# Kernel tuning notes

Measured on AMD Instinct MI355X. Metric: run time of the kernel, lower is better.

Reference implementation:

```python
import jax, jax.numpy as jnp
import numpy as np

B, S, D, H, DFF = 2, 2048, 2048, 16, 8192
DH = D // H
EPS = 1e-5


def _layer_norm(x, g, b):
    mu = jnp.mean(x, axis=-1, keepdims=True)
    var = jnp.mean(jnp.square(x - mu), axis=-1, keepdims=True)
    return (x - mu) * jax.lax.rsqrt(var + EPS) * g + b


def setup_inputs() -> dict:
    key = jax.random.key(0)
    ks = jax.random.split(key, 12)
    sc = 0.02
    inp = {
        "x": jax.random.normal(ks[0], (B, S, D), dtype=jnp.float32),
        # attention projections, stored [in, out] (torch Linear weight transposed)
        "wq": jax.random.normal(ks[1], (D, D), dtype=jnp.float32) * sc,
        "bq": jnp.zeros((D,), jnp.float32),
        "wk": jax.random.normal(ks[2], (D, D), dtype=jnp.float32) * sc,
        "bk": jnp.zeros((D,), jnp.float32),
        "wv": jax.random.normal(ks[3], (D, D), dtype=jnp.float32) * sc,
        "bv": jnp.zeros((D,), jnp.float32),
        "wo": jax.random.normal(ks[4], (D, D), dtype=jnp.float32) * sc,
        "bo": jnp.zeros((D,), jnp.float32),
        "ln1_g": jnp.ones((D,), jnp.float32),
        "ln1_b": jnp.zeros((D,), jnp.float32),
        # feed-forward
        "w1": jax.random.normal(ks[5], (D, DFF), dtype=jnp.float32) * sc,
        "b1": jnp.zeros((DFF,), jnp.float32),
        "w2": jax.random.normal(ks[6], (DFF, D), dtype=jnp.float32) * sc,
        "b2": jnp.zeros((D,), jnp.float32),
        "ln2_g": jnp.ones((D,), jnp.float32),
        "ln2_b": jnp.zeros((D,), jnp.float32),
    }
    return inp


def reference(x, wq, bq, wk, bk, wv, bv, wo, bo, ln1_g, ln1_b,
              w1, b1, w2, b2, ln2_g, ln2_b):
    # ---- MultiHeadAttentionBlock: x + MHA(LN(x)) ----
    h = _layer_norm(x, ln1_g, ln1_b)                      # [B,S,D]
    q = (h @ wq + bq).reshape(B, S, H, DH).transpose(0, 2, 1, 3)  # [B,H,S,DH]
    k = (h @ wk + bk).reshape(B, S, H, DH).transpose(0, 2, 1, 3)
    v = (h @ wv + bv).reshape(B, S, H, DH).transpose(0, 2, 1, 3)

    # faithful to source: scale by sqrt(d_dim), NOT sqrt(head_dim)
    scores = jnp.einsum("bhqd,bhkd->bhqk", q, k) / np.sqrt(D).astype(np.float32)
    # faithful triu/transpose masking (softmax sees raw zeros, not -inf)
    t = jnp.triu(scores).swapaxes(-2, -1)                 # [B,H,S,S]
    s = jax.nn.softmax(t, axis=-2)
    r = jnp.triu(s).swapaxes(-2, -1)
    attn = jnp.einsum("bhqk,bhkd->bhqd", r, v)            # [B,H,S,DH]
    attn = attn.transpose(0, 2, 1, 3).reshape(B, S, D)
    x = x + attn @ wo + bo

    # ---- FeedForwardBlock: x + FF(LN(x)), dropout rate 0 ----
    h2 = _layer_norm(x, ln2_g, ln2_b)
    ff = jax.nn.relu(h2 @ w1 + b1) @ w2 + b2
    return x + ff
```

## Files before the change

kernel.cpp:

```cpp
#include <hip/hip_runtime.h>


typedef unsigned short ushort_t;
typedef unsigned int   uint32;
typedef __attribute__((ext_vector_type(8))) short    short8;
typedef __attribute__((ext_vector_type(8))) ushort_t ushort8;
typedef __attribute__((ext_vector_type(4))) float    f32x4;

#define BDIM   2
#define SEQ    2048
#define DMODEL 2048
#define NHEAD  16
#define DHEAD  128
#define DFFN   8192
#define MROWS  (BDIM*SEQ)
#define LDQKV  6144

#define GPTR(p) (const __attribute__((address_space(1))) void*)((const void*)(p))
#define SPTR(p) (__attribute__((address_space(3))) void*)((void*)(p))

__device__ __forceinline__ float bf2f(ushort_t u) {
  union { uint32 i; float f; } c; c.i = ((uint32)u) << 16; return c.f;
}
__device__ __forceinline__ ushort_t f2bf(float f) {
  union { float f; uint32 i; } c; c.f = f;
  uint32 u = c.i;
  return (ushort_t)((u + 0x7fffu + ((u >> 16) & 1u)) >> 16);
}

__global__ __launch_bounds__(256) void transpose_f32_bf16_kern(
    const float* __restrict__ W, ushort_t* __restrict__ Wt, int K, int N)
{
  __shared__ float tile[32][33];
  const int nb = blockIdx.x * 32, kb = blockIdx.y * 32;
  const int tx = threadIdx.x & 31, ty = threadIdx.x >> 5;
#pragma unroll
  for (int j = 0; j < 32; j += 8)
    tile[ty + j][tx] = W[(size_t)(kb + ty + j) * N + nb + tx];
  __syncthreads();
#pragma unroll
  for (int j = 0; j < 32; j += 8)
    Wt[(size_t)(nb + ty + j) * K + kb + tx] = f2bf(tile[tx][ty + j]);
}

__global__ __launch_bounds__(256) void bias_concat_kern(
    const float* __restrict__ a, const float* __restrict__ b,
    const float* __restrict__ c, float* __restrict__ o)
{
  const int i = blockIdx.x * 256 + threadIdx.x;
  o[i] = (i < 2048) ? a[i] : ((i < 4096) ? b[i - 2048] : c[i - 4096]);
}

__global__ __launch_bounds__(256) void ln_kern(
    const float* __restrict__ X, const float* __restrict__ G,
    const float* __restrict__ Bb, ushort_t* __restrict__ Out)
{
  const int row = blockIdx.x, tid = threadIdx.x;
  const float* xr = X + (size_t)row * DMODEL;
  float4 v0 = ((const float4*)xr)[tid * 2];
  float4 v1 = ((const float4*)xr)[tid * 2 + 1];
  float s  = v0.x + v0.y + v0.z + v0.w + v1.x + v1.y + v1.z + v1.w;
  float ss = v0.x*v0.x + v0.y*v0.y + v0.z*v0.z + v0.w*v0.w
           + v1.x*v1.x + v1.y*v1.y + v1.z*v1.z + v1.w*v1.w;
#pragma unroll
  for (int off = 32; off > 0; off >>= 1) {
    s  += __shfl_down(s, off);
    ss += __shfl_down(ss, off);
  }
  __shared__ float rs[4], rss[4];
  __shared__ float sh_mu, sh_rst;
  const int wv = tid >> 6;
  if ((tid & 63) == 0) { rs[wv] = s; rss[wv] = ss; }
  __syncthreads();
  if (tid == 0) {
    float S1 = rs[0] + rs[1] + rs[2] + rs[3];
    float S2 = rss[0] + rss[1] + rss[2] + rss[3];
    float mu = S1 * (1.f / DMODEL);
    float var = S2 * (1.f / DMODEL) - mu * mu;
    sh_mu = mu;
    sh_rst = rsqrtf(var + 1e-5f);
  }
  __syncthreads();
  const float mu = sh_mu, rst = sh_rst;
  float4 g0 = ((const float4*)G)[tid * 2];
  float4 g1 = ((const float4*)G)[tid * 2 + 1];
  float4 b0 = ((const float4*)Bb)[tid * 2];
  float4 b1 = ((const float4*)Bb)[tid * 2 + 1];
  ushort8 o;
  o[0] = f2bf((v0.x - mu) * rst * g0.x + b0.x);
  o[1] = f2bf((v0.y - mu) * rst * g0.y + b0.y);
  o[2] = f2bf((v0.z - mu) * rst * g0.z + b0.z);
  o[3] = f2bf((v0.w - mu) * rst * g0.w + b0.w);
  o[4] = f2bf((v1.x - mu) * rst * g1.x + b1.x);
  o[5] = f2bf((v1.y - mu) * rst * g1.y + b1.y);
  o[6] = f2bf((v1.z - mu) * rst * g1.z + b1.z);
  o[7] = f2bf((v1.w - mu) * rst * g1.w + b1.w);
  *(ushort8*)(Out + (size_t)row * DMODEL + tid * 8) = o;
}

template<int OUT, int RELU, int RESID, int KDIV>
__global__ __launch_bounds__(512, 2) void gemm8_kern(
    const ushort_t* __restrict__ A, const ushort_t* __restrict__ Bt,
    const float* __restrict__ bias, const float* __restrict__ resid,
    void* __restrict__ Cout, int M, int N, int K)
{
  __shared__ ushort_t sA[4 * 8192];
  __shared__ ushort_t sB[4 * 8192];

  const int tid = threadIdx.x;
  const int nM  = gridDim.y;
  const int nwg = gridDim.x * nM;
  const int bid = blockIdx.y * gridDim.x + blockIdx.x;
  const int cpx = nwg >> 3;
  const int swz = (bid & 7) * cpx + (bid >> 3);
  const int m0 = (swz % nM) * 256;
  const int n0 = (swz / nM) * 256;

  const int Keff = K / KDIV;
  const int k0 = (KDIV > 1) ? blockIdx.z * Keff : 0;
  const int T = Keff >> 6;

  const int l = tid & 63, w = tid >> 6;
  const int lr = l & 15, lg = l >> 4;
  const int wr = w >> 2, wc = w & 3;

  const int xch   = (lg ^ ((lr >> 1) & 3)) * 8;
  const int abase = (wr * 128 + lr) * 32 + xch;
  const int bbase = (wc * 64  + lr) * 32 + xch;

  const int sr = tid >> 2;
  const int sg = ((tid & 3) ^ ((tid >> 3) & 3)) * 8;
  const ushort_t* Asrc = A  + (size_t)(m0 + sr) * K + k0 + sg;
  const ushort_t* Bsrc = Bt + (size_t)(n0 + sr) * K + k0 + sg;
  ushort_t* dA = sA + tid * 8;
  ushort_t* dB = sB + tid * 8;

#define SA_(slot, kt, kk, r) __builtin_amdgcn_global_load_lds( \
    GPTR(Asrc + (size_t)(r) * 128 * K + (kt) * 64 + (kk) * 32), \
    SPTR(dA + (slot) * 8192 + (r) * 4096), 16, 0, 0)
#define SB_(slot, kt, kk, r) __builtin_amdgcn_global_load_lds( \
    GPTR(Bsrc + (size_t)(r) * 128 * K + (kt) * 64 + (kk) * 32), \
    SPTR(dB + (slot) * 8192 + (r) * 4096), 16, 0, 0)

  f32x4 acc[8][4] = {};

  SA_(0, 0, 0, 0); SA_(0, 0, 0, 1); SB_(0, 0, 0, 0); SB_(0, 0, 0, 1);
  SA_(1, 0, 1, 0); SA_(1, 0, 1, 1); SB_(1, 0, 1, 0); SB_(1, 0, 1, 1);
  SA_(2, 1, 0, 0); SA_(2, 1, 0, 1); SB_(2, 1, 0, 0); SB_(2, 1, 0, 1);
  asm volatile("s_waitcnt vmcnt(8)" ::: "memory");
  __builtin_amdgcn_s_barrier();

  for (int t = 0; t < T; ++t) {
    const int c = t & 1;
    const ushort_t* A0 = sA + (c * 2 + 0) * 8192;
    const ushort_t* B0 = sB + (c * 2 + 0) * 8192;
    const ushort_t* A1 = sA + (c * 2 + 1) * 8192;
    const ushort_t* B1 = sB + (c * 2 + 1) * 8192;
    const int s1 = (c ^ 1) * 2 + 1;
    const int s0 = c * 2;
    const bool pf1 = (t + 1 < T), pf0 = (t + 2 < T);
    const bool last2 = (t >= T - 2);

    short8 a0, a1, a2, a3, b0, b1, b2, b3;

    b0 = *(const short8*)(B0 + bbase);
    b1 = *(const short8*)(B0 + bbase + 512);
    b2 = *(const short8*)(B0 + bbase + 1024);
    b3 = *(const short8*)(B0 + bbase + 1536);
    a0 = *(const short8*)(A0 + abase);
    a1 = *(const short8*)(A0 + abase + 512);
    a2 = *(const short8*)(A0 + abase + 1024);
    a3 = *(const short8*)(A0 + abase + 1536);
    if (pf1) { SA_(s1, t + 1, 1, 0); SA_(s1, t + 1, 1, 1); }
    __builtin_amdgcn_s_barrier();
    asm volatile("s_waitcnt lgkmcnt(0)" ::: "memory");
    __builtin_amdgcn_sched_barrier(0);
    __builtin_amdgcn_s_setprio(1);
    acc[0][0] = __builtin_amdgcn_mfma_f32_16x16x32_bf16(a0, b0, acc[0][0], 0, 0, 0);
    acc[0][1] = __builtin_amdgcn_mfma_f32_16x16x32_bf16(a0, b1, acc[0][1], 0, 0, 0);
    acc[0][2] = __builtin_amdgcn_mfma_f32_16x16x32_bf16(a0, b2, acc[0][2], 0, 0, 0);
    acc[0][3] = __builtin_amdgcn_mfma_f32_16x16x32_bf16(a0, b3, acc[0][3], 0, 0, 0);
    acc[1][0] = __builtin_amdgcn_mfma_f32_16x16x32_bf16(a1, b0, acc[1][0], 0, 0, 0);
    acc[1][1] = __builtin_amdgcn_mfma_f32_16x16x32_bf16(a1, b1, acc[1][1], 0, 0, 0);
    acc[1][2] = __builtin_amdgcn_mfma_f32_16x16x32_bf16(a1, b2, acc[1][2], 0, 0, 0);
    acc[1][3] = __builtin_amdgcn_mfma_f32_16x16x32_bf16(a1, b3, acc[1][3], 0, 0, 0);
    acc[2][0] = __builtin_amdgcn_mfma_f32_16x16x32_bf16(a2, b0, acc[2][0], 0, 0, 0);
    acc[2][1] = __builtin_amdgcn_mfma_f32_16x16x32_bf16(a2, b1, acc[2][1], 0, 0, 0);
    acc[2][2] = __builtin_amdgcn_mfma_f32_16x16x32_bf16(a2, b2, acc[2][2], 0, 0, 0);
    acc[2][3] = __builtin_amdgcn_mfma_f32_16x16x32_bf16(a2, b3, acc[2][3], 0, 0, 0);
    acc[3][0] = __builtin_amdgcn_mfma_f32_16x16x32_bf16(a3, b0, acc[3][0], 0, 0, 0);
    acc[3][1] = __builtin_amdgcn_mfma_f32_16x16x32_bf16(a3, b1, acc[3][1], 0, 0, 0);
    acc[3][2] = __builtin_amdgcn_mfma_f32_16x16x32_bf16(a3, b2, acc[3][2], 0, 0, 0);
    acc[3][3] = __builtin_amdgcn_mfma_f32_16x16x32_bf16(a3, b3, acc[3][3], 0, 0, 0);
    __builtin_amdgcn_s_setprio(0);
    __builtin_amdgcn_s_barrier();

    a0 = *(const short8*)(A0 + abase + 2048);
    a1 = *(const short8*)(A0 + abase + 2560);
    a2 = *(const short8*)(A0 + abase + 3072);
    a3 = *(const short8*)(A0 + abase + 3584);
    if (pf1) { SB_(s1, t + 1, 1, 0); SB_(s1, t + 1, 1, 1); }
    __builtin_amdgcn_s_barrier();
    asm volatile("s_waitcnt lgkmcnt(0)" ::: "memory");
    __builtin_amdgcn_sched_barrier(0);
    __builtin_amdgcn_s_setprio(1);
    acc[4][0] = __builtin_amdgcn_mfma_f32_16x16x32_bf16(a0, b0, acc[4][0], 0, 0, 0);
    acc[4][1] = __builtin_amdgcn_mfma_f32_16x16x32_bf16(a0, b1, acc[4][1], 0, 0, 0);
    acc[4][2] = __builtin_amdgcn_mfma_f32_16x16x32_bf16(a0, b2, acc[4][2], 0, 0, 0);
    acc[4][3] = __builtin_amdgcn_mfma_f32_16x16x32_bf16(a0, b3, acc[4][3], 0, 0, 0);
    acc[5][0] = __builtin_amdgcn_mfma_f32_16x16x32_bf16(a1, b0, acc[5][0], 0, 0, 0);
    acc[5][1] = __builtin_amdgcn_mfma_f32_16x16x32_bf16(a1, b1, acc[5][1], 0, 0, 0);
    acc[5][2] = __builtin_amdgcn_mfma_f32_16x16x32_bf16(a1, b2, acc[5][2], 0, 0, 0);
    acc[5][3] = __builtin_amdgcn_mfma_f32_16x16x32_bf16(a1, b3, acc[5][3], 0, 0, 0);
    acc[6][0] = __builtin_amdgcn_mfma_f32_16x16x32_bf16(a2, b0, acc[6][0], 0, 0, 0);
    acc[6][1] = __builtin_amdgcn_mfma_f32_16x16x32_bf16(a2, b1, acc[6][1], 0, 0, 0);
    acc[6][2] = __builtin_amdgcn_mfma_f32_16x16x32_bf16(a2, b2, acc[6][2], 0, 0, 0);
    acc[6][3] = __builtin_amdgcn_mfma_f32_16x16x32_bf16(a2, b3, acc[6][3], 0, 0, 0);
    acc[7][0] = __builtin_amdgcn_mfma_f32_16x16x32_bf16(a3, b0, acc[7][0], 0, 0, 0);
    acc[7][1] = __builtin_amdgcn_mfma_f32_16x16x32_bf16(a3, b1, acc[7][1], 0, 0, 0);
    acc[7][2] = __builtin_amdgcn_mfma_f32_16x16x32_bf16(a3, b2, acc[7][2], 0, 0, 0);
    acc[7][3] = __builtin_amdgcn_mfma_f32_16x16x32_bf16(a3, b3, acc[7][3], 0, 0, 0);
    __builtin_amdgcn_s_setprio(0);
    if (!last2) { asm volatile("s_waitcnt vmcnt(8)" ::: "memory"); }
    else        { asm volatile("s_waitcnt vmcnt(0)" ::: "memory"); }
    __builtin_amdgcn_s_barrier();

    b0 = *(const short8*)(B1 + bbase);
    b1 = *(const short8*)(B1 + bbase + 512);
    b2 = *(const short8*)(B1 + bbase + 1024);
    b3 = *(const short8*)(B1 + bbase + 1536);
    a0 = *(const short8*)(A1 + abase);
    a1 = *(const short8*)(A1 + abase + 512);
    a2 = *(const short8*)(A1 + abase + 1024);
    a3 = *(const short8*)(A1 + abase + 1536);
    if (pf0) { SA_(s0, t + 2, 0, 0); SA_(s0, t + 2, 0, 1); }
    __builtin_amdgcn_s_barrier();
    asm volatile("s_waitcnt lgkmcnt(0)" ::: "memory");
    __builtin_amdgcn_sched_barrier(0);
    __builtin_amdgcn_s_setprio(1);
    acc[0][0] = __builtin_amdgcn_mfma_f32_16x16x32_bf16(a0, b0, acc[0][0], 0, 0, 0);
    acc[0][1] = __builtin_amdgcn_mfma_f32_16x16x32_bf16(a0, b1, acc[0][1], 0, 0, 0);
    acc[0][2] = __builtin_amdgcn_mfma_f32_16x16x32_bf16(a0, b2, acc[0][2], 0, 0, 0);
    acc[0][3] = __builtin_amdgcn_mfma_f32_16x16x32_bf16(a0, b3, acc[0][3], 0, 0, 0);
    acc[1][0] = __builtin_amdgcn_mfma_f32_16x16x32_bf16(a1, b0, acc[1][0], 0, 0, 0);
    acc[1][1] = __builtin_amdgcn_mfma_f32_16x16x32_bf16(a1, b1, acc[1][1], 0, 0, 0);
    acc[1][2] = __builtin_amdgcn_mfma_f32_16x16x32_bf16(a1, b2, acc[1][2], 0, 0, 0);
    acc[1][3] = __builtin_amdgcn_mfma_f32_16x16x32_bf16(a1, b3, acc[1][3], 0, 0, 0);
    acc[2][0] = __builtin_amdgcn_mfma_f32_16x16x32_bf16(a2, b0, acc[2][0], 0, 0, 0);
    acc[2][1] = __builtin_amdgcn_mfma_f32_16x16x32_bf16(a2, b1, acc[2][1], 0, 0, 0);
    acc[2][2] = __builtin_amdgcn_mfma_f32_16x16x32_bf16(a2, b2, acc[2][2], 0, 0, 0);
    acc[2][3] = __builtin_amdgcn_mfma_f32_16x16x32_bf16(a2, b3, acc[2][3], 0, 0, 0);
    acc[3][0] = __builtin_amdgcn_mfma_f32_16x16x32_bf16(a3, b0, acc[3][0], 0, 0, 0);
    acc[3][1] = __builtin_amdgcn_mfma_f32_16x16x32_bf16(a3, b1, acc[3][1], 0, 0, 0);
    acc[3][2] = __builtin_amdgcn_mfma_f32_16x16x32_bf16(a3, b2, acc[3][2], 0, 0, 0);
    acc[3][3] = __builtin_amdgcn_mfma_f32_16x16x32_bf16(a3, b3, acc[3][3], 0, 0, 0);
    __builtin_amdgcn_s_setprio(0);
    __builtin_amdgcn_s_barrier();

    a0 = *(const short8*)(A1 + abase + 2048);
    a1 = *(const short8*)(A1 + abase + 2560);
    a2 = *(const short8*)(A1 + abase + 3072);
    a3 = *(const short8*)(A1 + abase + 3584);
    if (pf0) { SB_(s0, t + 2, 0, 0); SB_(s0, t + 2, 0, 1); }
    __builtin_amdgcn_s_barrier();
    asm volatile("s_waitcnt lgkmcnt(0)" ::: "memory");
    __builtin_amdgcn_sched_barrier(0);
    __builtin_amdgcn_s_setprio(1);
    acc[4][0] = __builtin_amdgcn_mfma_f32_16x16x32_bf16(a0, b0, acc[4][0], 0, 0, 0);
    acc[4][1] = __builtin_amdgcn_mfma_f32_16x16x32_bf16(a0, b1, acc[4][1], 0, 0, 0);
    acc[4][2] = __builtin_amdgcn_mfma_f32_16x16x32_bf16(a0, b2, acc[4][2], 0, 0, 0);
    acc[4][3] = __builtin_amdgcn_mfma_f32_16x16x32_bf16(a0, b3, acc[4][3], 0, 0, 0);
    acc[5][0] = __builtin_amdgcn_mfma_f32_16x16x32_bf16(a1, b0, acc[5][0], 0, 0, 0);
    acc[5][1] = __builtin_amdgcn_mfma_f32_16x16x32_bf16(a1, b1, acc[5][1], 0, 0, 0);
    acc[5][2] = __builtin_amdgcn_mfma_f32_16x16x32_bf16(a1, b2, acc[5][2], 0, 0, 0);
    acc[5][3] = __builtin_amdgcn_mfma_f32_16x16x32_bf16(a1, b3, acc[5][3], 0, 0, 0);
    acc[6][0] = __builtin_amdgcn_mfma_f32_16x16x32_bf16(a2, b0, acc[6][0], 0, 0, 0);
    acc[6][1] = __builtin_amdgcn_mfma_f32_16x16x32_bf16(a2, b1, acc[6][1], 0, 0, 0);
    acc[6][2] = __builtin_amdgcn_mfma_f32_16x16x32_bf16(a2, b2, acc[6][2], 0, 0, 0);
    acc[6][3] = __builtin_amdgcn_mfma_f32_16x16x32_bf16(a2, b3, acc[6][3], 0, 0, 0);
    acc[7][0] = __builtin_amdgcn_mfma_f32_16x16x32_bf16(a3, b0, acc[7][0], 0, 0, 0);
    acc[7][1] = __builtin_amdgcn_mfma_f32_16x16x32_bf16(a3, b1, acc[7][1], 0, 0, 0);
    acc[7][2] = __builtin_amdgcn_mfma_f32_16x16x32_bf16(a3, b2, acc[7][2], 0, 0, 0);
    acc[7][3] = __builtin_amdgcn_mfma_f32_16x16x32_bf16(a3, b3, acc[7][3], 0, 0, 0);
    __builtin_amdgcn_s_setprio(0);
    if (!last2) { asm volatile("s_waitcnt vmcnt(8)" ::: "memory"); }
    else        { asm volatile("s_waitcnt vmcnt(0)" ::: "memory"); }
    __builtin_amdgcn_s_barrier();
  }
#undef SA_
#undef SB_

  ushort_t* Pz = (OUT == 2)
      ? (ushort_t*)Cout + (size_t)blockIdx.z * M * N : (ushort_t*)Cout;
#pragma unroll
  for (int mi = 0; mi < 8; ++mi) {
#pragma unroll
    for (int ni = 0; ni < 4; ++ni) {
      const int gn = n0 + wc * 64 + ni * 16 + lr;
      const float bvv = (OUT == 2) ? 0.f : bias[gn];
#pragma unroll
      for (int j = 0; j < 4; ++j) {
        const int gm = m0 + wr * 128 + mi * 16 + lg * 4 + j;
        float v = acc[mi][ni][j] + bvv;
        if (RESID) v += resid[(size_t)gm * N + gn];
        if (RELU) v = fmaxf(v, 0.f);
        if (OUT == 0)      ((float*)Cout)[(size_t)gm * N + gn] = v;
        else               Pz[(size_t)gm * N + gn] = f2bf(v);
      }
    }
  }
}

__global__ __launch_bounds__(256) void combine_kern(
    const ushort_t* __restrict__ pp, const float* __restrict__ bias,
    const float* __restrict__ resid, float* __restrict__ out)
{
  const size_t i = ((size_t)blockIdx.x * 256 + threadIdx.x) * 8;
  ushort8 p0 = *(const ushort8*)(pp + i);
  ushort8 p1 = *(const ushort8*)(pp + (size_t)MROWS * 2048 + i);
  const int col = (int)(i & 2047);
  float4 r0 = *(const float4*)(resid + i);
  float4 r1 = *(const float4*)(resid + i + 4);
  float4 c0 = *(const float4*)(bias + col);
  float4 c1 = *(const float4*)(bias + col + 4);
  float4 o0, o1;
  o0.x = bf2f(p0[0]) + bf2f(p1[0]) + c0.x + r0.x;
  o0.y = bf2f(p0[1]) + bf2f(p1[1]) + c0.y + r0.y;
  o0.z = bf2f(p0[2]) + bf2f(p1[2]) + c0.z + r0.z;
  o0.w = bf2f(p0[3]) + bf2f(p1[3]) + c0.w + r0.w;
  o1.x = bf2f(p0[4]) + bf2f(p1[4]) + c1.x + r1.x;
  o1.y = bf2f(p0[5]) + bf2f(p1[5]) + c1.y + r1.y;
  o1.z = bf2f(p0[6]) + bf2f(p1[6]) + c1.z + r1.z;
  o1.w = bf2f(p0[7]) + bf2f(p1[7]) + c1.w + r1.w;
  *(float4*)(out + i) = o0;
  *(float4*)(out + i + 4) = o1;
}

__global__ __launch_bounds__(256) void attn_stats_kern(
    const ushort_t* __restrict__ Q, const ushort_t* __restrict__ Kb,
    float* __restrict__ E, float* __restrict__ DG, int ld)
{
  __shared__ ushort_t Ksm[64 * 128];
  const int qb = blockIdx.x;
  const int bh = blockIdx.y;
  const int b = bh >> 4, h = bh & 15;
  const int tid = threadIdx.x;
  const int l = tid & 63, w = tid >> 6;
  const int lr = l & 15, lg = l >> 4;

  const int qrow0 = qb * 64 + w * 16;

  const size_t qoff = (size_t)(b * SEQ + qrow0 + lr) * ld + h * DHEAD + lg * 8;
  short8 af[4];
#pragma unroll
  for (int c = 0; c < 4; ++c) af[c] = *(const short8*)(Q + qoff + c * 32);

  const int srow_b = w * 16 + (l >> 4);
  const ushort_t* Kg = Kb + (size_t)b * SEQ * ld + (size_t)h * DHEAD;
  ushort_t* Sbase = Ksm + w * 2048;

  f32x4 sume = {0.f, 0.f, 0.f, 0.f};
  f32x4 dge  = {0.f, 0.f, 0.f, 0.f};
  const float scale = 0.0220970869120796f;
  const int rx = lr & 7;

  for (int kc = qb; kc < 32; ++kc) {
    __syncthreads();
#pragma unroll
    for (int c = 0; c < 4; ++c) {
      const int row = srow_b + c * 4;
      const int g = (l & 15) ^ (row & 7);
      __builtin_amdgcn_global_load_lds(
          GPTR(Kg + (size_t)(kc * 64 + row) * ld + g * 8),
          SPTR(Sbase + c * 512), 16, 0, 0);
    }
    __syncthreads();

    const int ks0 = (kc == qb) ? w : 0;
    for (int ks = ks0; ks < 4; ++ks) {
      short8 bfr[4];
#pragma unroll
      for (int c = 0; c < 4; ++c)
        bfr[c] = *(const short8*)(Ksm + (ks * 16 + lr) * 128 + ((lg + c * 4) ^ rx) * 8);
      f32x4 sc = {0.f, 0.f, 0.f, 0.f};
      sc = __builtin_amdgcn_mfma_f32_16x16x32_bf16(af[0], bfr[0], sc, 0, 0, 0);
      sc = __builtin_amdgcn_mfma_f32_16x16x32_bf16(af[1], bfr[1], sc, 0, 0, 0);
      sc = __builtin_amdgcn_mfma_f32_16x16x32_bf16(af[2], bfr[2], sc, 0, 0, 0);
      sc = __builtin_amdgcn_mfma_f32_16x16x32_bf16(af[3], bfr[3], sc, 0, 0, 0);
      if (kc == qb && ks == w) {
        const int ki = kc * 64 + ks * 16 + lr;
#pragma unroll
        for (int j = 0; j < 4; ++j) {
          const int qi = qrow0 + lg * 4 + j;
          if (ki >= qi) {
            float e = __expf(sc[j] * scale);
            sume[j] += e;
            if (ki == qi) dge[j] += e;
          }
        }
      } else {
#pragma unroll
        for (int j = 0; j < 4; ++j)
          sume[j] += __expf(sc[j] * scale);
      }
    }
  }

#pragma unroll
  for (int j = 0; j < 4; ++j) {
#pragma unroll
    for (int off = 1; off < 16; off <<= 1) {
      sume[j] += __shfl_xor(sume[j], off);
      dge[j]  += __shfl_xor(dge[j], off);
    }
  }
  if (lr == 0) {
#pragma unroll
    for (int j = 0; j < 4; ++j) {
      E[(size_t)bh * SEQ + qrow0 + lg * 4 + j]  = sume[j];
      DG[(size_t)bh * SEQ + qrow0 + lg * 4 + j] = dge[j];
    }
  }
}

__global__ __launch_bounds__(128) void vchunk_kern(
    const ushort_t* __restrict__ V, float* __restrict__ CS, int ld)
{
  const int c = blockIdx.x, bh = blockIdx.y;
  const int b = bh >> 4, h = bh & 15;
  const int dh = threadIdx.x;
  const ushort_t* vp = V + (size_t)(b * SEQ + c * 64) * ld + h * DHEAD + dh;
  float s = 0.f;
  for (int i = 0; i < 64; ++i) s += bf2f(vp[(size_t)i * ld]);
  CS[((size_t)bh * 32 + c) * 128 + dh] = s;
}

__global__ __launch_bounds__(128) void attn_combine_kern(
    const ushort_t* __restrict__ V, const float* __restrict__ CS,
    const float* __restrict__ E, const float* __restrict__ DG,
    ushort_t* __restrict__ Attn, int ldv)
{
  const int c = blockIdx.x, bh = blockIdx.y;
  const int b = bh >> 4, h = bh & 15;
  const int dh = threadIdx.x;
  float prefix = 0.f;
  for (int cc = 0; cc < c; ++cc) prefix += CS[((size_t)bh * 32 + cc) * 128 + dh];
  const ushort_t* vp = V + (size_t)(b * SEQ + c * 64) * ldv + h * DHEAD + dh;
  ushort_t* ap = Attn + (size_t)(b * SEQ + c * 64) * DMODEL + h * DHEAD + dh;
  const int qb = c * 64;
  for (int i = 0; i < 64; ++i) {
    const int qq = qb + i;
    const float denom = (float)qq + E[(size_t)bh * SEQ + qq];
    const float de = DG[(size_t)bh * SEQ + qq];
    const float vv = bf2f(vp[(size_t)i * ldv]);
    ap[(size_t)i * DMODEL] = f2bf((prefix + de * vv) / denom);
    prefix += vv;
  }
}

extern "C" void kernel_launch(void* const* d_in, const int* in_sizes, int n_in,
                              void* d_out, int out_size, void* d_ws, size_t ws_size,
                              hipStream_t stream)
{
  const float* x    = (const float*)d_in[0];
  const float* wq   = (const float*)d_in[1];
  const float* bq   = (const float*)d_in[2];
  const float* wk   = (const float*)d_in[3];
  const float* bk   = (const float*)d_in[4];
  const float* wv   = (const float*)d_in[5];
  const float* bv   = (const float*)d_in[6];
  const float* wo   = (const float*)d_in[7];
  const float* bo   = (const float*)d_in[8];
  const float* ln1g = (const float*)d_in[9];
  const float* ln1b = (const float*)d_in[10];
  const float* w1   = (const float*)d_in[11];
  const float* b1   = (const float*)d_in[12];
  const float* w2   = (const float*)d_in[13];
  const float* b2   = (const float*)d_in[14];
  const float* ln2g = (const float*)d_in[15];
  const float* ln2b = (const float*)d_in[16];
  float* out = (float*)d_out;

  char* ws = (char*)d_ws;
  ushort_t* W1T  = (ushort_t*)(ws + 0);
  ushort_t* PPf2 = (ushort_t*)(ws + 0);
  ushort_t* W2T  = (ushort_t*)(ws + 33554432);
  ushort_t* WOT  = (ushort_t*)(ws + 67108864);
  float*    X2   = (float*)   (ws + 75497472);
  float*    Bcat = (float*)   (ws + 75497472);
  ushort_t* Hb   = (ushort_t*)(ws + 109051904);
  ushort_t* F1   = (ushort_t*)(ws + 125829120);
  ushort_t* PPwo = (ushort_t*)(ws + 125829120);
  ushort_t* WQKV = (ushort_t*)(ws + 125829120);
  ushort_t* QKVb = (ushort_t*)(ws + 150994944);
  float*    Eb   = (float*)   (ws + 201326592);
  float*    DGb  = (float*)   (ws + 201588736);
  float*    CSb  = (float*)   (ws + 201850880);

  transpose_f32_bf16_kern<<<dim3(64, 64),  256, 0, stream>>>(wq, WQKV,                   2048, 2048);
  transpose_f32_bf16_kern<<<dim3(64, 64),  256, 0, stream>>>(wk, WQKV + 2048 * 2048,     2048, 2048);
  transpose_f32_bf16_kern<<<dim3(64, 64),  256, 0, stream>>>(wv, WQKV + 2 * 2048 * 2048, 2048, 2048);
  transpose_f32_bf16_kern<<<dim3(64, 64),  256, 0, stream>>>(wo, WOT, 2048, 2048);
  transpose_f32_bf16_kern<<<dim3(256, 64), 256, 0, stream>>>(w1, W1T, 2048, 8192);
  transpose_f32_bf16_kern<<<dim3(64, 256), 256, 0, stream>>>(w2, W2T, 8192, 2048);
  bias_concat_kern<<<24, 256, 0, stream>>>(bq, bk, bv, Bcat);

  ln_kern<<<MROWS, 256, 0, stream>>>(x, ln1g, ln1b, Hb);

  gemm8_kern<1, 0, 0, 1><<<dim3(24, 16), 512, 0, stream>>>(
      Hb, WQKV, Bcat, nullptr, QKVb, MROWS, LDQKV, DMODEL);

  attn_stats_kern<<<dim3(32, 32), 256, 0, stream>>>(QKVb, QKVb + 2048, Eb, DGb, LDQKV);

  vchunk_kern<<<dim3(32, 32), 128, 0, stream>>>(QKVb + 4096, CSb, LDQKV);
  attn_combine_kern<<<dim3(32, 32), 128, 0, stream>>>(QKVb + 4096, CSb, Eb, DGb, Hb, LDQKV);

  gemm8_kern<2, 0, 0, 2><<<dim3(8, 16, 2), 512, 0, stream>>>(
      Hb, WOT, bo, nullptr, PPwo, MROWS, DMODEL, DMODEL);
  combine_kern<<<4096, 256, 0, stream>>>(PPwo, bo, x, X2);

  ln_kern<<<MROWS, 256, 0, stream>>>(X2, ln2g, ln2b, Hb);

  gemm8_kern<1, 1, 0, 1><<<dim3(32, 16), 512, 0, stream>>>(
      Hb, W1T, b1, nullptr, F1, MROWS, DFFN, DMODEL);

  gemm8_kern<2, 0, 0, 2><<<dim3(8, 16, 2), 512, 0, stream>>>(
      F1, W2T, b2, nullptr, PPf2, MROWS, DMODEL, DFFN);
  combine_kern<<<4096, 256, 0, stream>>>(PPf2, b2, X2, out);
}
```

Before: 687.3 us.

## Fuse weight prep launches, fuse combine with LN2, widen attention-stats query tiles

Merges the six weight transpose launches and the bias concat into a single prep kernel. Fuses the split-K combine for the output projection with the second layer norm, so X2 is not re-read. The attention-stats kernel now processes 128 query rows per block, two 16-row groups per wave, so each loaded K tile is reused for twice as many queries. It also drops the sched_barrier calls in the GEMM main loop, which gives the compiler freedom to reorder but may disturb the hand-tuned interleaving.

```diff
diff --git a/kernel.cpp b/kernel.cpp
--- a/kernel.cpp
+++ b/kernel.cpp
@@ -3,9 +3,9 @@
 
 typedef unsigned short ushort_t;
 typedef unsigned int   uint32;
-typedef __attribute__((ext_vector_type(8))) short    short8;
-typedef __attribute__((ext_vector_type(8))) ushort_t ushort8;
-typedef __attribute__((ext_vector_type(4))) float    f32x4;
+typedef __attribute__((ext_vector_type(8)))  short    short8;
+typedef __attribute__((ext_vector_type(8)))  ushort_t ushort8;
+typedef __attribute__((ext_vector_type(4)))  float    f32x4;
 
 #define BDIM   2
 #define SEQ    2048
@@ -28,11 +28,34 @@
   return (ushort_t)((u + 0x7fffu + ((u >> 16) & 1u)) >> 16);
 }
 
-__global__ __launch_bounds__(256) void transpose_f32_bf16_kern(
-    const float* __restrict__ W, ushort_t* __restrict__ Wt, int K, int N)
-{
+__global__ __launch_bounds__(256) void prep_kern(
+    const float* __restrict__ wq, const float* __restrict__ wk,
+    const float* __restrict__ wv, const float* __restrict__ wo,
+    const float* __restrict__ w1, const float* __restrict__ w2,
+    const float* __restrict__ bq, const float* __restrict__ bk,
+    const float* __restrict__ bv,
+    ushort_t* __restrict__ WQKV, ushort_t* __restrict__ WOT,
+    ushort_t* __restrict__ W1T, ushort_t* __restrict__ W2T,
+    float* __restrict__ Bcat)
+{
+  const int bid = blockIdx.x;
+  if (bid >= 49152) {
+    for (int i = threadIdx.x; i < 6144; i += 256)
+      Bcat[i] = (i < 2048) ? bq[i] : ((i < 4096) ? bk[i - 2048] : bv[i - 4096]);
+    return;
+  }
+  const float* W; ushort_t* Wt; int K, N, local;
+  if (bid < 12288) {
+    const int which = bid >> 12; local = bid & 4095;
+    W = (which == 0) ? wq : (which == 1) ? wk : wv;
+    Wt = WQKV + (size_t)which * 2048 * 2048; K = 2048; N = 2048;
+  } else if (bid < 16384) { W = wo; Wt = WOT; K = 2048; N = 2048; local = bid - 12288; }
+  else if (bid < 32768)   { W = w1; Wt = W1T; K = 2048; N = 8192; local = bid - 16384; }
+  else                    { W = w2; Wt = W2T; K = 8192; N = 2048; local = bid - 32768; }
+  const int ntiles = N >> 5;
+  const int nb = (local % ntiles) * 32, kb = (local / ntiles) * 32;
+
   __shared__ float tile[32][33];
-  const int nb = blockIdx.x * 32, kb = blockIdx.y * 32;
   const int tx = threadIdx.x & 31, ty = threadIdx.x >> 5;
 #pragma unroll
   for (int j = 0; j < 32; j += 8)
@@ -41,14 +64,6 @@
 #pragma unroll
   for (int j = 0; j < 32; j += 8)
     Wt[(size_t)(nb + ty + j) * K + kb + tx] = f2bf(tile[tx][ty + j]);
-}
-
-__global__ __launch_bounds__(256) void bias_concat_kern(
-    const float* __restrict__ a, const float* __restrict__ b,
-    const float* __restrict__ c, float* __restrict__ o)
-{
-  const int i = blockIdx.x * 256 + threadIdx.x;
-  o[i] = (i < 2048) ? a[i] : ((i < 4096) ? b[i - 2048] : c[i - 4096]);
 }
 
 __global__ __launch_bounds__(256) void ln_kern(
@@ -98,11 +113,58 @@
   *(ushort8*)(Out + (size_t)row * DMODEL + tid * 8) = o;
 }
 
-template<int OUT, int RELU, int RESID, int KDIV>
+__global__ __launch_bounds__(256) void combine_ln_kern(
+    const ushort_t* __restrict__ pp, const float* __restrict__ bias,
+    const float* __restrict__ xres, const float* __restrict__ G,
+    const float* __restrict__ Bb, float* __restrict__ X2,
+    ushort_t* __restrict__ Out)
+{
+  const int row = blockIdx.x, tid = threadIdx.x;
+  const size_t i = (size_t)row * DMODEL + tid * 8;
+  ushort8 p0 = *(const ushort8*)(pp + i);
+  ushort8 p1 = *(const ushort8*)(pp + (size_t)MROWS * 2048 + i);
+  float v[8];
+#pragma unroll
+  for (int j = 0; j < 8; ++j)
+    v[j] = bf2f(p0[j]) + bf2f(p1[j]) + bias[tid * 8 + j] + xres[i + j];
+  float4 o0 = {v[0], v[1], v[2], v[3]}, o1 = {v[4], v[5], v[6], v[7]};
+  *(float4*)(X2 + i) = o0;
+  *(float4*)(X2 + i + 4) = o1;
+
+  float s = 0.f, ss = 0.f;
+#pragma unroll
+  for (int j = 0; j < 8; ++j) { s += v[j]; ss += v[j] * v[j]; }
+#pragma unroll
+  for (int off = 32; off > 0; off >>= 1) {
+    s  += __shfl_down(s, off);
+    ss += __shfl_down(ss, off);
+  }
+  __shared__ float rs[4], rss[4];
+  __shared__ float sh_mu, sh_rst;
+  const int wvv = tid >> 6;
+  if ((tid & 63) == 0) { rs[wvv] = s; rss[wvv] = ss; }
+  __syncthreads();
+  if (tid == 0) {
+    float S1 = rs[0] + rs[1] + rs[2] + rs[3];
+    float S2 = rss[0] + rss[1] + rss[2] + rss[3];
+    float mu = S1 * (1.f / DMODEL);
+    float var = S2 * (1.f / DMODEL) - mu * mu;
+    sh_mu = mu; sh_rst = rsqrtf(var + 1e-5f);
+  }
+  __syncthreads();
+  const float mu = sh_mu, rst = sh_rst;
+  ushort8 o;
+#pragma unroll
+  for (int j = 0; j < 8; ++j)
+    o[j] = f2bf((v[j] - mu) * rst * G[tid * 8 + j] + Bb[tid * 8 + j]);
+  *(ushort8*)(Out + i) = o;
+}
+
+template<int OUT, int RELU, int KDIV>
 __global__ __launch_bounds__(512, 2) void gemm8_kern(
     const ushort_t* __restrict__ A, const ushort_t* __restrict__ Bt,
-    const float* __restrict__ bias, const float* __restrict__ resid,
-    void* __restrict__ Cout, int M, int N, int K)
+    const float* __restrict__ bias, void* __restrict__ Cout,
+    int M, int N, int K)
 {
   __shared__ ushort_t sA[4 * 8192];
   __shared__ ushort_t sB[4 * 8192];
@@ -174,7 +236,6 @@
     if (pf1) { SA_(s1, t + 1, 1, 0); SA_(s1, t + 1, 1, 1); }
     __builtin_amdgcn_s_barrier();
     asm volatile("s_waitcnt lgkmcnt(0)" ::: "memory");
-    __builtin_amdgcn_sched_barrier(0);
     __builtin_amdgcn_s_setprio(1);
     acc[0][0] = __builtin_amdgcn_mfma_f32_16x16x32_bf16(a0, b0, acc[0][0], 0, 0, 0);
     acc[0][1] = __builtin_amdgcn_mfma_f32_16x16x32_bf16(a0, b1, acc[0][1], 0, 0, 0);
@@ -202,7 +263,6 @@
     if (pf1) { SB_(s1, t + 1, 1, 0); SB_(s1, t + 1, 1, 1); }
     __builtin_amdgcn_s_barrier();
     asm volatile("s_waitcnt lgkmcnt(0)" ::: "memory");
-    __builtin_amdgcn_sched_barrier(0);
     __builtin_amdgcn_s_setprio(1);
     acc[4][0] = __builtin_amdgcn_mfma_f32_16x16x32_bf16(a0, b0, acc[4][0], 0, 0, 0);
     acc[4][1] = __builtin_amdgcn_mfma_f32_16x16x32_bf16(a0, b1, acc[4][1], 0, 0, 0);
@@ -236,7 +296,6 @@
     if (pf0) { SA_(s0, t + 2, 0, 0); SA_(s0, t + 2, 0, 1); }
     __builtin_amdgcn_s_barrier();
     asm volatile("s_waitcnt lgkmcnt(0)" ::: "memory");
-    __builtin_amdgcn_sched_barrier(0);
     __builtin_amdgcn_s_setprio(1);
     acc[0][0] = __builtin_amdgcn_mfma_f32_16x16x32_bf16(a0, b0, acc[0][0], 0, 0, 0);
     acc[0][1] = __builtin_amdgcn_mfma_f32_16x16x32_bf16(a0, b1, acc[0][1], 0, 0, 0);
@@ -264,7 +323,6 @@
     if (pf0) { SB_(s0, t + 2, 0, 0); SB_(s0, t + 2, 0, 1); }
     __builtin_amdgcn_s_barrier();
     asm volatile("s_waitcnt lgkmcnt(0)" ::: "memory");
-    __builtin_amdgcn_sched_barrier(0);
     __builtin_amdgcn_s_setprio(1);
     acc[4][0] = __builtin_amdgcn_mfma_f32_16x16x32_bf16(a0, b0, acc[4][0], 0, 0, 0);
     acc[4][1] = __builtin_amdgcn_mfma_f32_16x16x32_bf16(a0, b1, acc[4][1], 0, 0, 0);
@@ -302,10 +360,8 @@
       for (int j = 0; j < 4; ++j) {
         const int gm = m0 + wr * 128 + mi * 16 + lg * 4 + j;
         float v = acc[mi][ni][j] + bvv;
-        if (RESID) v += resid[(size_t)gm * N + gn];
         if (RELU) v = fmaxf(v, 0.f);
-        if (OUT == 0)      ((float*)Cout)[(size_t)gm * N + gn] = v;
-        else               Pz[(size_t)gm * N + gn] = f2bf(v);
+        Pz[(size_t)gm * N + gn] = f2bf(v);
       }
     }
   }
@@ -348,23 +404,26 @@
   const int l = tid & 63, w = tid >> 6;
   const int lr = l & 15, lg = l >> 4;
 
-  const int qrow0 = qb * 64 + w * 16;
-
-  const size_t qoff = (size_t)(b * SEQ + qrow0 + lr) * ld + h * DHEAD + lg * 8;
-  short8 af[4];
-#pragma unroll
-  for (int c = 0; c < 4; ++c) af[c] = *(const short8*)(Q + qoff + c * 32);
+  const int qrow0 = qb * 128 + w * 32;
+
+  short8 af[2][4];
+#pragma unroll
+  for (int g = 0; g < 2; ++g) {
+    const size_t qoff = (size_t)(b * SEQ + qrow0 + g * 16 + lr) * ld + h * DHEAD + lg * 8;
+#pragma unroll
+    for (int c = 0; c < 4; ++c) af[g][c] = *(const short8*)(Q + qoff + c * 32);
+  }
 
   const int srow_b = w * 16 + (l >> 4);
   const ushort_t* Kg = Kb + (size_t)b * SEQ * ld + (size_t)h * DHEAD;
   ushort_t* Sbase = Ksm + w * 2048;
 
-  f32x4 sume = {0.f, 0.f, 0.f, 0.f};
-  f32x4 dge  = {0.f, 0.f, 0.f, 0.f};
+  f32x4 sume[2] = {{0.f,0.f,0.f,0.f},{0.f,0.f,0.f,0.f}};
+  f32x4 dge[2]  = {{0.f,0.f,0.f,0.f},{0.f,0.f,0.f,0.f}};
   const float scale = 0.0220970869120796f;
   const int rx = lr & 7;
 
-  for (int kc = qb; kc < 32; ++kc) {
+  for (int kc = qb * 2; kc < 32; ++kc) {
     __syncthreads();
 #pragma unroll
     for (int c = 0; c < 4; ++c) {
@@ -376,50 +435,61 @@
     }
     __syncthreads();
 
-    const int ks0 = (kc == qb) ? w : 0;
-    for (int ks = ks0; ks < 4; ++ks) {
+    for (int ks = 0; ks < 4; ++ks) {
+      const int kbase = kc * 64 + ks * 16;
+      if (kbase + 16 <= qrow0) continue;
       short8 bfr[4];
 #pragma unroll
       for (int c = 0; c < 4; ++c)
         bfr[c] = *(const short8*)(Ksm + (ks * 16 + lr) * 128 + ((lg + c * 4) ^ rx) * 8);
-      f32x4 sc = {0.f, 0.f, 0.f, 0.f};
-      sc = __builtin_amdgcn_mfma_f32_16x16x32_bf16(af[0], bfr[0], sc, 0, 0, 0);
-      sc = __builtin_amdgcn_mfma_f32_16x16x32_bf16(af[1], bfr[1], sc, 0, 0, 0);
-      sc = __builtin_amdgcn_mfma_f32_16x16x32_bf16(af[2], bfr[2], sc, 0, 0, 0);
-      sc = __builtin_amdgcn_mfma_f32_16x16x32_bf16(af[3], bfr[3], sc, 0, 0, 0);
-      if (kc == qb && ks == w) {
-        const int ki = kc * 64 + ks * 16 + lr;
-#pragma unroll
-        for (int j = 0; j < 4; ++j) {
-          const int qi = qrow0 + lg * 4 + j;
-          if (ki >= qi) {
-            float e = __expf(sc[j] * scale);
-            sume[j] += e;
-            if (ki == qi) dge[j] += e;
+#pragma unroll
+      for (int g = 0; g < 2; ++g) {
+        const int qg = qrow0 + g * 16;
+        if (kbase < qg) continue;
+        f32x4 sc = {0.f, 0.f, 0.f, 0.f};
+        sc = __builtin_amdgcn_mfma_f32_16x16x32_bf16(af[g][0], bfr[0], sc, 0, 0, 0);
+        sc = __builtin_amdgcn_mfma_f32_16x16x32_bf16(af[g][1], bfr[1], sc, 0, 0, 0);
+        sc = __builtin_amdgcn_mfma_f32_16x16x32_bf16(af[g][2], bfr[2], sc, 0, 0, 0);
+        sc = __builtin_amdgcn_mfma_f32_16x16x32_bf16(af[g][3], bfr[3], sc, 0, 0, 0);
+        if (kbase == qg) {
+          const int ki = kbase + lr;
+#pragma unroll
+          for (int j = 0; j < 4; ++j) {
+            const int qi = qg + lg * 4 + j;
+            if (ki >= qi) {
+              float e = __expf(sc[j] * scale);
+              sume[g][j] += e;
+              if (ki == qi) dge[g][j] += e;
+            }
           }
+        } else {
+#pragma unroll
+          for (int j = 0; j < 4; ++j)
+            sume[g][j] += __expf(sc[j] * scale);
         }
-      } else {
-#pragma unroll
-        for (int j = 0; j < 4; ++j)
-          sume[j] += __expf(sc[j] * scale);
       }
     }
   }
 
 #pragma unroll
-  for (int j = 0; j < 4; ++j) {
-#pragma unroll
-    for (int off = 1; off < 16; off <<= 1) {
-      sume[j] += __shfl_xor(sume[j], off);
-      dge[j]  += __shfl_xor(dge[j], off);
+  for (int g = 0; g < 2; ++g) {
+#pragma unroll
+    for (int j = 0; j < 4; ++j) {
+#pragma unroll
+      for (int off = 1; off < 16; off <<= 1) {
+        sume[g][j] += __shfl_xor(sume[g][j], off);
+        dge[g][j]  += __shfl_xor(dge[g][j], off);
+      }
     }
   }
   if (lr == 0) {
 #pragma unroll
-    for (int j = 0; j < 4; ++j) {
-      E[(size_t)bh * SEQ + qrow0 + lg * 4 + j]  = sume[j];
-      DG[(size_t)bh * SEQ + qrow0 + lg * 4 + j] = dge[j];
-    }
+    for (int g = 0; g < 2; ++g)
+#pragma unroll
+      for (int j = 0; j < 4; ++j) {
+        E[(size_t)bh * SEQ + qrow0 + g * 16 + lg * 4 + j]  = sume[g][j];
+        DG[(size_t)bh * SEQ + qrow0 + g * 16 + lg * 4 + j] = dge[g][j];
+      }
   }
 }
 
@@ -497,34 +567,28 @@
   float*    DGb  = (float*)   (ws + 201588736);
   float*    CSb  = (float*)   (ws + 201850880);
 
-  transpose_f32_bf16_kern<<<dim3(64, 64),  256, 0, stream>>>(wq, WQKV,                   2048, 2048);
-  transpose_f32_bf16_kern<<<dim3(64, 64),  256, 0, stream>>>(wk, WQKV + 2048 * 2048,     2048, 2048);
-  transpose_f32_bf16_kern<<<dim3(64, 64),  256, 0, stream>>>(wv, WQKV + 2 * 2048 * 2048, 2048, 2048);
-  transpose_f32_bf16_kern<<<dim3(64, 64),  256, 0, stream>>>(wo, WOT, 2048, 2048);
-  transpose_f32_bf16_kern<<<dim3(256, 64), 256, 0, stream>>>(w1, W1T, 2048, 8192);
-  transpose_f32_bf16_kern<<<dim3(64, 256), 256, 0, stream>>>(w2, W2T, 8192, 2048);
-  bias_concat_kern<<<24, 256, 0, stream>>>(bq, bk, bv, Bcat);
+  prep_kern<<<49153, 256, 0, stream>>>(wq, wk, wv, wo, w1, w2, bq, bk, bv,
+                                       WQKV, WOT, W1T, W2T, Bcat);
 
   ln_kern<<<MROWS, 256, 0, stream>>>(x, ln1g, ln1b, Hb);
 
-  gemm8_kern<1, 0, 0, 1><<<dim3(24, 16), 512, 0, stream>>>(
-      Hb, WQKV, Bcat, nullptr, QKVb, MROWS, LDQKV, DMODEL);
-
-  attn_stats_kern<<<dim3(32, 32), 256, 0, stream>>>(QKVb, QKVb + 2048, Eb, DGb, LDQKV);
+  gemm8_kern<1, 0, 1><<<dim3(24, 16), 512, 0, stream>>>(
+      Hb, WQKV, Bcat, QKVb, MROWS, LDQKV, DMODEL);
+
+  attn_stats_kern<<<dim3(16, 32), 256, 0, stream>>>(QKVb, QKVb + 2048, Eb, DGb, LDQKV);
 
   vchunk_kern<<<dim3(32, 32), 128, 0, stream>>>(QKVb + 4096, CSb, LDQKV);
   attn_combine_kern<<<dim3(32, 32), 128, 0, stream>>>(QKVb + 4096, CSb, Eb, DGb, Hb, LDQKV);
 
-  gemm8_kern<2, 0, 0, 2><<<dim3(8, 16, 2), 512, 0, stream>>>(
-      Hb, WOT, bo, nullptr, PPwo, MROWS, DMODEL, DMODEL);
-  combine_kern<<<4096, 256, 0, stream>>>(PPwo, bo, x, X2);
-
-  ln_kern<<<MROWS, 256, 0, stream>>>(X2, ln2g, ln2b, Hb);
-
-  gemm8_kern<1, 1, 0, 1><<<dim3(32, 16), 512, 0, stream>>>(
-      Hb, W1T, b1, nullptr, F1, MROWS, DFFN, DMODEL);
-
-  gemm8_kern<2, 0, 0, 2><<<dim3(8, 16, 2), 512, 0, stream>>>(
-      F1, W2T, b2, nullptr, PPf2, MROWS, DMODEL, DFFN);
+  gemm8_kern<2, 0, 2><<<dim3(8, 16, 2), 512, 0, stream>>>(
+      Hb, WOT, bo, PPwo, MROWS, DMODEL, DMODEL);
+
+  combine_ln_kern<<<MROWS, 256, 0, stream>>>(PPwo, bo, x, ln2g, ln2b, X2, Hb);
+
+  gemm8_kern<1, 1, 1><<<dim3(32, 16), 512, 0, stream>>>(
+      Hb, W1T, b1, F1, MROWS, DFFN, DMODEL);
+
+  gemm8_kern<2, 0, 2><<<dim3(8, 16, 2), 512, 0, stream>>>(
+      F1, W2T, b2, PPf2, MROWS, DMODEL, DFFN);
   combine_kern<<<4096, 256, 0, stream>>>(PPf2, b2, X2, out);
 }
```

Result: faster. 661.0 us (-3.8%).
